# Performance work log

Measured on AMD Instinct MI355X. Metric: run time of the kernel, lower is better.

## Reference

```python
import jax, jax.numpy as jnp
import numpy as np

B, L = 128, 4096
H, RH, D, K = 128, 64, 64, 512  # num_hiddens, residual_hiddens, embedding_dim, num_embeddings
BETA = 0.25  # commitment_cost


def conv1d(x, w, b=None, stride=1, pad=0):
    # x: (N, C, W); w: (O, I, K) torch layout
    y = jax.lax.conv_general_dilated(x, w, (stride,), [(pad, pad)],
                                     dimension_numbers=('NCW', 'OIW', 'NCW'))
    return y if b is None else y + b[None, :, None]


def convT1d(x, w, b=None, stride=2, pad=1):
    # torch ConvTranspose1d weight layout (in, out, k)
    k = w.shape[-1]
    w_t = jnp.flip(w, -1).transpose(1, 0, 2)  # (out, in, k)
    y = jax.lax.conv_general_dilated(x, w_t, (1,), [(k - 1 - pad, k - 1 - pad)],
                                     lhs_dilation=(stride,),
                                     dimension_numbers=('NCW', 'OIW', 'NCW'))
    return y if b is None else y + b[None, :, None]


def res_stack(x, layers):
    for w1, w2 in layers:
        h = conv1d(jax.nn.relu(x), w1, None, 1, 1)
        h = conv1d(jax.nn.relu(h), w2, None, 1, 0)
        x = x + h
    return jax.nn.relu(x)


def _forward(x, enc_w1, enc_b1, enc_w2, enc_b2, enc_w3, enc_b3,
             enc_r1a, enc_r1b, enc_r2a, enc_r2b, pre_vq_w, pre_vq_b, codebook,
             dec_w1, dec_b1, dec_r1a, dec_r1b, dec_r2a, dec_r2b,
             dec_ct1_w, dec_ct1_b, dec_ct2_w, dec_ct2_b):
    # ---- Encoder (compression_factor == 4) ----
    h = x[:, None, :]                                   # (B, 1, L)
    h = jax.nn.relu(conv1d(h, enc_w1, enc_b1, 2, 1))    # (B, H/2, L/2)
    h = jax.nn.relu(conv1d(h, enc_w2, enc_b2, 2, 1))    # (B, H, L/4)
    h = conv1d(h, enc_w3, enc_b3, 1, 1)
    h = res_stack(h, [(enc_r1a, enc_r1b), (enc_r2a, enc_r2b)])
    z = conv1d(h, pre_vq_w, pre_vq_b, 1, 0)             # (B, D, T)

    # ---- Vector quantization ----
    zt = z.transpose(0, 2, 1)                           # (B, T, D)
    flat = zt.reshape(-1, D)                            # (BT, D)
    dists = (jnp.sum(flat * flat, 1, keepdims=True)
             - 2.0 * flat @ codebook.T
             + jnp.sum(codebook * codebook, 1))         # (BT, K)
    idx = jnp.argmin(dists, axis=1)                     # (BT,)
    q = codebook[idx].reshape(zt.shape)                 # (B, T, D)

    e_latent = jnp.mean((jax.lax.stop_gradient(q) - zt) ** 2)
    q_latent = jnp.mean((q - jax.lax.stop_gradient(zt)) ** 2)
    loss = q_latent + BETA * e_latent
    q_st = zt + jax.lax.stop_gradient(q - zt)           # straight-through

    counts = jnp.zeros((K,), flat.dtype).at[idx].add(1.0)
    probs = counts / idx.shape[0]
    perplexity = jnp.exp(-jnp.sum(probs * jnp.log(probs + 1e-10)))

    # ---- Decoder (compression_factor == 4) ----
    hd = q_st.transpose(0, 2, 1)                        # (B, D, T)
    hd = conv1d(hd, dec_w1, dec_b1, 1, 1)               # (B, H, T)
    hd = res_stack(hd, [(dec_r1a, dec_r1b), (dec_r2a, dec_r2b)])
    hd = jax.nn.relu(convT1d(hd, dec_ct1_w, dec_ct1_b)) # (B, H/2, 2T)
    hd = convT1d(hd, dec_ct2_w, dec_ct2_b)              # (B, 1, 4T)
    recon = jnp.squeeze(hd)                             # (B, L)
    return loss, recon, perplexity


def setup_inputs() -> dict:
    key = jax.random.key(0)
    ks = jax.random.split(key, 32)
    n = lambda i, shape, s=0.05: jax.random.normal(ks[i], shape, jnp.float32) * s
    inp = {
        'x': jax.random.normal(ks[0], (B, L), jnp.float32),
        'enc_w1': n(1, (H // 2, 1, 4)), 'enc_b1': jnp.zeros((H // 2,), jnp.float32),
        'enc_w2': n(2, (H, H // 2, 4)), 'enc_b2': jnp.zeros((H,), jnp.float32),
        'enc_w3': n(3, (H, H, 3)), 'enc_b3': jnp.zeros((H,), jnp.float32),
        'enc_r1a': n(4, (RH, H, 3)), 'enc_r1b': n(5, (H, RH, 1)),
        'enc_r2a': n(6, (RH, H, 3)), 'enc_r2b': n(7, (H, RH, 1)),
        'pre_vq_w': n(8, (D, H, 1)), 'pre_vq_b': jnp.zeros((D,), jnp.float32),
        'codebook': jax.random.uniform(ks[9], (K, D), jnp.float32, -1.0 / K, 1.0 / K),
        'dec_w1': n(10, (H, D, 3)), 'dec_b1': jnp.zeros((H,), jnp.float32),
        'dec_r1a': n(11, (RH, H, 3)), 'dec_r1b': n(12, (H, RH, 1)),
        'dec_r2a': n(13, (RH, H, 3)), 'dec_r2b': n(14, (H, RH, 1)),
        'dec_ct1_w': n(15, (H, H // 2, 4)), 'dec_ct1_b': jnp.zeros((H // 2,), jnp.float32),
        'dec_ct2_w': n(16, (H // 2, 1, 4)), 'dec_ct2_b': jnp.zeros((1,), jnp.float32),
    }
    return inp


def reference(x, enc_w1, enc_b1, enc_w2, enc_b2, enc_w3, enc_b3,
              enc_r1a, enc_r1b, enc_r2a, enc_r2b, pre_vq_w, pre_vq_b, codebook,
              dec_w1, dec_b1, dec_r1a, dec_r1b, dec_r2a, dec_r2b,
              dec_ct1_w, dec_ct1_b, dec_ct2_w, dec_ct2_b):
    return _forward(x, enc_w1, enc_b1, enc_w2, enc_b2, enc_w3, enc_b3,
                    enc_r1a, enc_r1b, enc_r2a, enc_r2b, pre_vq_w, pre_vq_b, codebook,
                    dec_w1, dec_b1, dec_r1a, dec_r1b, dec_r2a, dec_r2b,
                    dec_ct1_w, dec_ct1_b, dec_ct2_w, dec_ct2_b)
```

## Files before the change

### kernel.cpp

```cpp
#include <hip/hip_runtime.h>
#include <hip/hip_bf16.h>
#include <math.h>

using bf16 = __hip_bfloat16;
typedef __attribute__((ext_vector_type(4))) float f32x4;
typedef __attribute__((ext_vector_type(8))) short s16x8;

#define MFMA16(a,b,c) __builtin_amdgcn_mfma_f32_16x16x32_bf16((a),(b),(c),0,0,0)


__device__ inline float bf2f(unsigned short u) {
    union { float f; unsigned v; } c; c.v = ((unsigned)u) << 16; return c.f;
}
__device__ inline unsigned short bfbits(float f) {
    union { bf16 h; unsigned short u; } c; c.h = __float2bfloat16(f); return c.u;
}
__device__ inline s16x8 relu8(s16x8 v) {
#pragma unroll
    for (int j = 0; j < 8; ++j)
        v[j] = (short)(((unsigned short)v[j] & 0x8000u) ? 0 : (unsigned short)v[j]);
    return v;
}

enum { M_S1 = 0, M_S2 = 1, M_CT = 2 };

template<int CIN, int COUT, int NTAP, int MODE, bool RELU_IN, bool RELU_OUT,
         bool HAS_BIAS>
__global__ __launch_bounds__(256) void gconv_k(
    const bf16* __restrict__ in, const bf16* __restrict__ wt,
    const float* __restrict__ bias, bf16* __restrict__ out,
    int Lin, int Lout)
{
    constexpr int T  = (MODE == M_S2) ? 132 : ((MODE == M_CT) ? 66 : (NTAP == 3 ? 66 : 64));
    constexpr int NG = (MODE == M_CT) ? 2 : 1;
    constexpr int WL = (COUT == 128) ? 4 : 2;
    constexpr int KS = CIN / 32;
    constexpr int SOFF = (MODE == M_CT || NTAP == 3) ? -1 : 0;
    __shared__ bf16 sX[T * CIN];

    const int tid = threadIdx.x;
    const int b   = blockIdx.y;
    const int l0  = blockIdx.x * 64;
    const bf16* inb = in + (size_t)b * Lin * CIN;

    constexpr int CPR = CIN / 8;
    for (int i = tid; i < T * CPR; i += 256) {
        int t  = i / CPR;
        int c0 = (i - t * CPR) * 8;
        int g;
        if (MODE == M_S2) g = (t < 66) ? 2 * (l0 + t) : 2 * (l0 + t - 66) - 1;
        else              g = l0 + t + SOFF;
        s16x8 v = {};
        if (g >= 0 && g < Lin) v = *(const s16x8*)(inb + (size_t)g * CIN + c0);
        if (RELU_IN) v = relu8(v);
        int byte = ((t * CIN + c0) << 1) ^ ((t & 7) << 4);
        *(s16x8*)((char*)sX + byte) = v;
    }
    __syncthreads();

    const int lane = tid & 63;
    const int wid  = __builtin_amdgcn_readfirstlane(tid >> 6);
    const int co0  = (COUT == 128) ? wid * 32 : (wid & 1) * 32;
    const int lw0  = (COUT == 128) ? 0 : (wid >> 1) * 32;
    const int lr   = lane & 15;
    const int kg   = lane >> 4;

    f32x4 acc[NG][2][WL];
#pragma unroll
    for (int g = 0; g < NG; ++g)
#pragma unroll
        for (int cf = 0; cf < 2; ++cf)
#pragma unroll
            for (int lf = 0; lf < WL; ++lf)
                acc[g][cf][lf] = (f32x4){0.f, 0.f, 0.f, 0.f};

#pragma unroll
    for (int g = 0; g < NG; ++g) {
#pragma unroll
        for (int k = 0; k < NTAP; ++k) {
            int roff;
            if (MODE == M_S1)      roff = k;
            else if (MODE == M_S2) roff = (k == 0) ? 66 : (k == 1) ? 0 : (k == 2) ? 67 : 1;
            else                   roff = g + k;
            const bf16* Ab = wt + (size_t)(g * NTAP + k) * COUT * CIN;
#pragma unroll
            for (int ks = 0; ks < KS; ++ks) {
                s16x8 af[2];
#pragma unroll
                for (int cf = 0; cf < 2; ++cf)
                    af[cf] = *(const s16x8*)(Ab + (co0 + cf * 16 + lr) * CIN + ks * 32 + kg * 8);
                s16x8 bfr[WL];
#pragma unroll
                for (int lf = 0; lf < WL; ++lf) {
                    int t = roff + lw0 + lf * 16 + lr;
                    int byte = ((t * CIN + ks * 32 + kg * 8) << 1) ^ ((t & 7) << 4);
                    bfr[lf] = *(const s16x8*)((const char*)sX + byte);
                }
#pragma unroll
                for (int cf = 0; cf < 2; ++cf)
#pragma unroll
                    for (int lf = 0; lf < WL; ++lf)
                        acc[g][cf][lf] = MFMA16(af[cf], bfr[lf], acc[g][cf][lf]);
            }
        }
    }

#pragma unroll
    for (int g = 0; g < NG; ++g)
#pragma unroll
        for (int cf = 0; cf < 2; ++cf)
#pragma unroll
            for (int lf = 0; lf < WL; ++lf) {
                int cb0  = co0 + cf * 16 + kg * 4;
                int lcol = lw0 + lf * 16 + lr;
                int gcol = (MODE == M_CT) ? (2 * (l0 + lcol) + g) : (l0 + lcol);
                float r[4];
#pragma unroll
                for (int j = 0; j < 4; ++j) {
                    r[j] = acc[g][cf][lf][j];
                    if (HAS_BIAS) r[j] += bias[cb0 + j];
                    if (RELU_OUT) r[j] = fmaxf(r[j], 0.f);
                }
                bf16* po = out + ((size_t)b * Lout + gcol) * COUT + cb0;
                uint2 pk;
                pk.x = (unsigned)bfbits(r[0]) | ((unsigned)bfbits(r[1]) << 16);
                pk.y = (unsigned)bfbits(r[2]) | ((unsigned)bfbits(r[3]) << 16);
                *(uint2*)po = pk;
            }
}

template<bool RELU_OUT>
__global__ __launch_bounds__(256) void fres_k(
    const bf16* __restrict__ in, const bf16* __restrict__ w1t,
    const bf16* __restrict__ w2t, bf16* __restrict__ out)
{
    __shared__ bf16 sX[66 * 128];
    __shared__ bf16 sH[64 * 64];
    const int tid = threadIdx.x;
    const int b   = blockIdx.y;
    const int l0  = blockIdx.x * 64;
    const bf16* inb = in + (size_t)b * 1024 * 128;

    for (int i = tid; i < 66 * 16; i += 256) {
        int t = i >> 4, c0 = (i & 15) * 8;
        int g = l0 + t - 1;
        s16x8 v = {};
        if (g >= 0 && g < 1024) v = *(const s16x8*)(inb + (size_t)g * 128 + c0);
        int byte = ((t * 128 + c0) << 1) ^ ((t & 7) << 4);
        *(s16x8*)((char*)sX + byte) = v;
    }
    __syncthreads();

    const int lane = tid & 63;
    const int wid  = __builtin_amdgcn_readfirstlane(tid >> 6);
    const int lr   = lane & 15;
    const int kg   = lane >> 4;

    {
        const int co0 = (wid & 1) * 32;
        const int lw0 = (wid >> 1) * 32;
        f32x4 acc[2][2];
#pragma unroll
        for (int cf = 0; cf < 2; ++cf)
#pragma unroll
            for (int lf = 0; lf < 2; ++lf) acc[cf][lf] = (f32x4){0.f, 0.f, 0.f, 0.f};
#pragma unroll
        for (int k = 0; k < 3; ++k) {
            const bf16* Ab = w1t + (size_t)k * 64 * 128;
#pragma unroll
            for (int ks = 0; ks < 4; ++ks) {
                s16x8 af[2];
#pragma unroll
                for (int cf = 0; cf < 2; ++cf)
                    af[cf] = *(const s16x8*)(Ab + (co0 + cf * 16 + lr) * 128 + ks * 32 + kg * 8);
                s16x8 bfr[2];
#pragma unroll
                for (int lf = 0; lf < 2; ++lf) {
                    int t = k + lw0 + lf * 16 + lr;
                    int byte = ((t * 128 + ks * 32 + kg * 8) << 1) ^ ((t & 7) << 4);
                    bfr[lf] = relu8(*(const s16x8*)((const char*)sX + byte));
                }
#pragma unroll
                for (int cf = 0; cf < 2; ++cf)
#pragma unroll
                    for (int lf = 0; lf < 2; ++lf)
                        acc[cf][lf] = MFMA16(af[cf], bfr[lf], acc[cf][lf]);
            }
        }
#pragma unroll
        for (int cf = 0; cf < 2; ++cf)
#pragma unroll
            for (int lf = 0; lf < 2; ++lf) {
                int pos = lw0 + lf * 16 + lr;
                int ch  = co0 + cf * 16 + kg * 4;
                uint2 pk;
                pk.x = (unsigned)bfbits(fmaxf(acc[cf][lf][0], 0.f)) |
                       ((unsigned)bfbits(fmaxf(acc[cf][lf][1], 0.f)) << 16);
                pk.y = (unsigned)bfbits(fmaxf(acc[cf][lf][2], 0.f)) |
                       ((unsigned)bfbits(fmaxf(acc[cf][lf][3], 0.f)) << 16);
                int byte = ((pos * 64 + ch) << 1) ^ ((pos & 7) << 4);
                *(uint2*)((char*)sH + byte) = pk;
            }
    }
    __syncthreads();

    {
        const int co0 = wid * 32;
        f32x4 acc2[2][4];
#pragma unroll
        for (int cf = 0; cf < 2; ++cf)
#pragma unroll
            for (int lf = 0; lf < 4; ++lf) acc2[cf][lf] = (f32x4){0.f, 0.f, 0.f, 0.f};
#pragma unroll
        for (int ks = 0; ks < 2; ++ks) {
            s16x8 af[2];
#pragma unroll
            for (int cf = 0; cf < 2; ++cf)
                af[cf] = *(const s16x8*)(w2t + (size_t)(co0 + cf * 16 + lr) * 64 + ks * 32 + kg * 8);
            s16x8 bfr[4];
#pragma unroll
            for (int lf = 0; lf < 4; ++lf) {
                int t = lf * 16 + lr;
                int byte = ((t * 64 + ks * 32 + kg * 8) << 1) ^ ((t & 7) << 4);
                bfr[lf] = *(const s16x8*)((const char*)sH + byte);
            }
#pragma unroll
            for (int cf = 0; cf < 2; ++cf)
#pragma unroll
                for (int lf = 0; lf < 4; ++lf)
                    acc2[cf][lf] = MFMA16(af[cf], bfr[lf], acc2[cf][lf]);
        }
#pragma unroll
        for (int cf = 0; cf < 2; ++cf)
#pragma unroll
            for (int lf = 0; lf < 4; ++lf) {
                int cb0  = co0 + cf * 16 + kg * 4;
                int lcol = lf * 16 + lr;
                int tX   = lcol + 1;
                int rbyte = ((tX * 128 + cb0) << 1) ^ ((tX & 7) << 4);
                uint2 old = *(const uint2*)((const char*)sX + rbyte);
                float r[4];
                r[0] = acc2[cf][lf][0] + bf2f((unsigned short)(old.x & 0xffff));
                r[1] = acc2[cf][lf][1] + bf2f((unsigned short)(old.x >> 16));
                r[2] = acc2[cf][lf][2] + bf2f((unsigned short)(old.y & 0xffff));
                r[3] = acc2[cf][lf][3] + bf2f((unsigned short)(old.y >> 16));
                if (RELU_OUT)
#pragma unroll
                    for (int j = 0; j < 4; ++j) r[j] = fmaxf(r[j], 0.f);
                uint2 pk;
                pk.x = (unsigned)bfbits(r[0]) | ((unsigned)bfbits(r[1]) << 16);
                pk.y = (unsigned)bfbits(r[2]) | ((unsigned)bfbits(r[3]) << 16);
                *(uint2*)(out + ((size_t)b * 1024 + l0 + lcol) * 128 + cb0) = pk;
            }
    }
}

__global__ __launch_bounds__(256) void enc1_k(
    const float* __restrict__ x, const float* __restrict__ w,
    const float* __restrict__ bias, bf16* __restrict__ out)
{
    const int tid = threadIdx.x;
    const int b   = blockIdx.y;
    const int l   = blockIdx.x * 256 + tid;
    const float* xb = x + (size_t)b * 4096;
    float xv[4];
#pragma unroll
    for (int k = 0; k < 4; ++k) {
        int g = 2 * l - 1 + k;
        xv[k] = (g >= 0 && g < 4096) ? xb[g] : 0.f;
    }
    bf16* ob = out + ((size_t)b * 2048 + l) * 64;
#pragma unroll
    for (int c0 = 0; c0 < 64; c0 += 8) {
        union { unsigned short u[8]; s16x8 v; } pk;
#pragma unroll
        for (int j = 0; j < 8; ++j) {
            int co = c0 + j;
            float a = bias[co];
#pragma unroll
            for (int k = 0; k < 4; ++k) a = fmaf(xv[k], w[co * 4 + k], a);
            pk.u[j] = bfbits(fmaxf(a, 0.f));
        }
        *(s16x8*)(ob + c0) = pk.v;
    }
}

__global__ __launch_bounds__(256) void ct2_k(
    const bf16* __restrict__ in, const float* __restrict__ w,
    const float* __restrict__ bias, float* __restrict__ out)
{
    __shared__ bf16 sX[258 * 64];
    const int tid = threadIdx.x;
    const int b   = blockIdx.y;
    const int m0  = blockIdx.x * 256;
    const bf16* inb = in + (size_t)b * 2048 * 64;
    for (int i = tid; i < 258 * 8; i += 256) {
        int t = i >> 3, c0 = (i & 7) * 8;
        int g = m0 - 1 + t;
        s16x8 v = {};
        if (g >= 0 && g < 2048) v = *(const s16x8*)(inb + (size_t)g * 64 + c0);
        int byte = ((t * 64 + c0) << 1) ^ ((t & 7) << 4);
        *(s16x8*)((char*)sX + byte) = v;
    }
    __syncthreads();
    float e = bias[0], o = bias[0];
#pragma unroll
    for (int c0 = 0; c0 < 64; c0 += 8) {
        int t0 = tid, t1 = tid + 1, t2 = tid + 2;
        s16x8 vm1 = *(const s16x8*)((char*)sX + (((t0 * 64 + c0) << 1) ^ ((t0 & 7) << 4)));
        s16x8 v0  = *(const s16x8*)((char*)sX + (((t1 * 64 + c0) << 1) ^ ((t1 & 7) << 4)));
        s16x8 vp1 = *(const s16x8*)((char*)sX + (((t2 * 64 + c0) << 1) ^ ((t2 & 7) << 4)));
#pragma unroll
        for (int j = 0; j < 8; ++j) {
            int ci = c0 + j;
            float xm1 = bf2f((unsigned short)vm1[j]);
            float x0  = bf2f((unsigned short)v0[j]);
            float xp1 = bf2f((unsigned short)vp1[j]);
            e = fmaf(x0,  w[ci * 4 + 1], fmaf(xm1, w[ci * 4 + 3], e));
            o = fmaf(xp1, w[ci * 4 + 0], fmaf(x0,  w[ci * 4 + 2], o));
        }
    }
    int m = m0 + tid;
    out[(size_t)b * 4096 + 2 * m]     = e;
    out[(size_t)b * 4096 + 2 * m + 1] = o;
}

__global__ __launch_bounds__(256) void wx_k(
    const float* ew2, const float* ew3, const float* er1a, const float* er1b,
    const float* er2a, const float* er2b, const float* pvw, const float* dw1,
    const float* dr1a, const float* dr1b, const float* dr2a, const float* dr2b,
    const float* ct1w, bf16* wb)
{
    const int job = blockIdx.x;
    bf16* dst = wb + (size_t)job * 65536;
    const float* src; int CO, CI, K;
    switch (job) {
        case 0:  src = ew2;  CO = 128; CI = 64;  K = 4; break;
        case 1:  src = ew3;  CO = 128; CI = 128; K = 3; break;
        case 2:  src = er1a; CO = 64;  CI = 128; K = 3; break;
        case 3:  src = er1b; CO = 128; CI = 64;  K = 1; break;
        case 4:  src = er2a; CO = 64;  CI = 128; K = 3; break;
        case 5:  src = er2b; CO = 128; CI = 64;  K = 1; break;
        case 6:  src = pvw;  CO = 64;  CI = 128; K = 1; break;
        case 7:  src = dw1;  CO = 128; CI = 64;  K = 3; break;
        case 8:  src = dr1a; CO = 64;  CI = 128; K = 3; break;
        case 9:  src = dr1b; CO = 128; CI = 64;  K = 1; break;
        case 10: src = dr2a; CO = 64;  CI = 128; K = 3; break;
        case 11: src = dr2b; CO = 128; CI = 64;  K = 1; break;
        default: src = ct1w; CO = 64;  CI = 128; K = 4; break;
    }
    const int tot = CO * CI * K;
    for (int i = blockIdx.y * 256 + threadIdx.x; i < tot; i += gridDim.y * 256) {
        if (job < 12) {
            int k = i / (CO * CI); int r = i - k * CO * CI;
            int co = r / CI; int ci = r - co * CI;
            dst[i] = __float2bfloat16(src[((size_t)co * CI + ci) * K + k]);
        } else {
            const int TAP[4] = {3, 1, 2, 0};
            int g = i / (64 * 128); int r = i - g * 64 * 128;
            int co = r / 128; int ci = r - co * 128;
            dst[i] = __float2bfloat16(src[((size_t)ci * 64 + co) * 4 + TAP[g]]);
        }
    }
}

__global__ __launch_bounds__(256) void cbprep_k(
    const float* __restrict__ cb, bf16* __restrict__ cbh, bf16* __restrict__ cbl,
// ... 175 lines not shown
        float4 q1 = *(const float4*)(qp + c0 + 4);
        float qv[8] = {q0.x, q0.y, q0.z, q0.w, q1.x, q1.y, q1.z, q1.w};
        float zv[8] = {z0.x, z0.y, z0.z, z0.w, z1.x, z1.y, z1.z, z1.w};
        union { unsigned short u[8]; s16x8 v; } pk;
#pragma unroll
        for (int j = 0; j < 8; ++j) {
            float d = qv[j] - zv[j];
            lsum = fmaf(d, d, lsum);
            pk.u[j] = bfbits(qv[j]);
        }
        *(s16x8*)(q + (size_t)n * 64 + c0) = pk.v;
    }
#pragma unroll
    for (int off = 32; off > 0; off >>= 1) lsum += __shfl_down(lsum, off, 64);
    if ((tid & 63) == 0) sWS[tid >> 6] = lsum;
    __syncthreads();
    if (tid == 0) atomicAdd(loss_sum, sWS[0] + sWS[1] + sWS[2] + sWS[3]);
    float c0v = sHist[tid];       if (c0v != 0.f) atomicAdd(&counts[tid], c0v);
    float c1v = sHist[tid + 256]; if (c1v != 0.f) atomicAdd(&counts[tid + 256], c1v);
}

__global__ __launch_bounds__(512) void finalize_k(
    const float* __restrict__ counts, const float* __restrict__ loss_sum,
    float* __restrict__ d_out, int out_size)
{
    __shared__ float ws2[8];
    const int tid = threadIdx.x;
    float p = counts[tid] * (1.f / 131072.f);
    float e = p * logf(p + 1e-10f);
#pragma unroll
    for (int off = 32; off > 0; off >>= 1) e += __shfl_down(e, off, 64);
    const int lane = tid & 63, wid = tid >> 6;
    if (lane == 0) ws2[wid] = e;
    __syncthreads();
    if (tid == 0) {
        float s = 0.f;
        for (int i = 0; i < 8; ++i) s += ws2[i];
        d_out[0] = 1.25f * loss_sum[0] * (1.f / 8388608.f);
        d_out[out_size - 1] = expf(-s);
    }
}

extern "C" void kernel_launch(void* const* d_in, const int* in_sizes, int n_in,
                              void* d_out, int out_size, void* d_ws, size_t ws_size,
                              hipStream_t stream)
{
    const float* x        = (const float*)d_in[0];
    const float* enc_w1   = (const float*)d_in[1];
    const float* enc_b1   = (const float*)d_in[2];
    const float* enc_b2   = (const float*)d_in[4];
    const float* enc_b3   = (const float*)d_in[6];
    const float* pre_vq_b = (const float*)d_in[12];
    const float* cb       = (const float*)d_in[13];
    const float* dec_b1   = (const float*)d_in[15];
    const float* ct1_b    = (const float*)d_in[21];
    const float* ct2_w    = (const float*)d_in[22];
    const float* ct2_b    = (const float*)d_in[23];
    float* out = (float*)d_out;

    char* base = (char*)d_ws;
    bf16*  wb   = (bf16*)base;
    bf16*  Abf  = (bf16*)(base + ((size_t)2   << 20));
    bf16*  Bbf  = (bf16*)(base + ((size_t)40  << 20));
    bf16*  Qbf  = (bf16*)(base + ((size_t)78  << 20));
    bf16*  cbh  = (bf16*)(base + ((size_t)96  << 20));
    bf16*  cbl  = (bf16*)(base + ((size_t)96  << 20) + 65536);
    float* sc   = (float*)(base + ((size_t)96  << 20) + 131072);
    float* cnt  = sc + 512;
    float* lsum = cnt + 512;

    hipMemsetAsync(cnt, 0, 513 * sizeof(float), stream);

    dim3 blk(256);
    dim3 g16(16, 128);

    wx_k<<<dim3(13, 8), blk, 0, stream>>>(
        (const float*)d_in[3], (const float*)d_in[5], (const float*)d_in[7],
        (const float*)d_in[8], (const float*)d_in[9], (const float*)d_in[10],
        (const float*)d_in[11], (const float*)d_in[14], (const float*)d_in[16],
        (const float*)d_in[17], (const float*)d_in[18], (const float*)d_in[19],
        (const float*)d_in[20], wb);
    cbprep_k<<<2, blk, 0, stream>>>(cb, cbh, cbl, sc);

    enc1_k<<<dim3(8, 128), blk, 0, stream>>>(x, enc_w1, enc_b1, Abf);
    gconv_k<64,128,4,M_S2,false,true ,true ><<<g16, blk, 0, stream>>>(
        Abf, wb + 0 * 65536, enc_b2, Bbf, 2048, 1024);
    gconv_k<128,128,3,M_S1,false,false,true ><<<g16, blk, 0, stream>>>(
        Bbf, wb + 1 * 65536, enc_b3, Abf, 1024, 1024);
    fres_k<false><<<g16, blk, 0, stream>>>(Abf, wb + 2 * 65536, wb + 3 * 65536, Bbf);
    fres_k<true ><<<g16, blk, 0, stream>>>(Bbf, wb + 4 * 65536, wb + 5 * 65536, Abf);

    vqf_k<<<512, blk, 0, stream>>>(Abf, wb + 6 * 65536, pre_vq_b, cb,
                                   cbh, cbl, sc, Qbf, cnt, lsum);

    gconv_k<64,128,3,M_S1,false,false,true ><<<g16, blk, 0, stream>>>(
        Qbf, wb + 7 * 65536, dec_b1, Abf, 1024, 1024);
    fres_k<false><<<g16, blk, 0, stream>>>(Abf, wb + 8 * 65536, wb + 9 * 65536, Bbf);
    fres_k<true ><<<g16, blk, 0, stream>>>(Bbf, wb + 10 * 65536, wb + 11 * 65536, Abf);
    gconv_k<128,64,2,M_CT,false,true ,true ><<<g16, blk, 0, stream>>>(
        Abf, wb + 12 * 65536, ct1_b, Bbf, 1024, 2048);

    ct2_k<<<dim3(8, 128), blk, 0, stream>>>(Bbf, ct2_w, ct2_b, out + 1);
    finalize_k<<<1, 512, 0, stream>>>(cnt, lsum, out, out_size);
}
```

Measured before the change: 418.1 us.

## Fuse encoder and decoder conv/residual chains into halo-tiled megakernels

```diff
diff --git a/kernel.cpp b/kernel.cpp
--- a/kernel.cpp
+++ b/kernel.cpp
@@ -22,128 +22,23 @@
     return v;
 }
 
-enum { M_S1 = 0, M_S2 = 1, M_CT = 2 };
-
-template<int CIN, int COUT, int NTAP, int MODE, bool RELU_IN, bool RELU_OUT,
-         bool HAS_BIAS>
-__global__ __launch_bounds__(256) void gconv_k(
-    const bf16* __restrict__ in, const bf16* __restrict__ wt,
-    const float* __restrict__ bias, bf16* __restrict__ out,
-    int Lin, int Lout)
+__global__ __launch_bounds__(256) void encmid_k(
+    const bf16* __restrict__ in, const bf16* __restrict__ w3t,
+    const float* __restrict__ b3, const bf16* __restrict__ r1w1,
+    const bf16* __restrict__ r1w2, const bf16* __restrict__ r2w1,
+    const bf16* __restrict__ r2w2, bf16* __restrict__ out)
 {
-    constexpr int T  = (MODE == M_S2) ? 132 : ((MODE == M_CT) ? 66 : (NTAP == 3 ? 66 : 64));
-    constexpr int NG = (MODE == M_CT) ? 2 : 1;
-    constexpr int WL = (COUT == 128) ? 4 : 2;
-    constexpr int KS = CIN / 32;
-    constexpr int SOFF = (MODE == M_CT || NTAP == 3) ? -1 : 0;
-    __shared__ bf16 sX[T * CIN];
-
-    const int tid = threadIdx.x;
-    const int b   = blockIdx.y;
-    const int l0  = blockIdx.x * 64;
-    const bf16* inb = in + (size_t)b * Lin * CIN;
-
-    constexpr int CPR = CIN / 8;
-    for (int i = tid; i < T * CPR; i += 256) {
-        int t  = i / CPR;
-        int c0 = (i - t * CPR) * 8;
-        int g;
-        if (MODE == M_S2) g = (t < 66) ? 2 * (l0 + t) : 2 * (l0 + t - 66) - 1;
-        else              g = l0 + t + SOFF;
-        s16x8 v = {};
-        if (g >= 0 && g < Lin) v = *(const s16x8*)(inb + (size_t)g * CIN + c0);
-        if (RELU_IN) v = relu8(v);
-        int byte = ((t * CIN + c0) << 1) ^ ((t & 7) << 4);
-        *(s16x8*)((char*)sX + byte) = v;
-    }
-    __syncthreads();
-
-    const int lane = tid & 63;
-    const int wid  = __builtin_amdgcn_readfirstlane(tid >> 6);
-    const int co0  = (COUT == 128) ? wid * 32 : (wid & 1) * 32;
-    const int lw0  = (COUT == 128) ? 0 : (wid >> 1) * 32;
-    const int lr   = lane & 15;
-    const int kg   = lane >> 4;
-
-    f32x4 acc[NG][2][WL];
-#pragma unroll
-    for (int g = 0; g < NG; ++g)
-#pragma unroll
-        for (int cf = 0; cf < 2; ++cf)
-#pragma unroll
-            for (int lf = 0; lf < WL; ++lf)
-                acc[g][cf][lf] = (f32x4){0.f, 0.f, 0.f, 0.f};
-
-#pragma unroll
-    for (int g = 0; g < NG; ++g) {
-#pragma unroll
-        for (int k = 0; k < NTAP; ++k) {
-            int roff;
-            if (MODE == M_S1)      roff = k;
-            else if (MODE == M_S2) roff = (k == 0) ? 66 : (k == 1) ? 0 : (k == 2) ? 67 : 1;
-            else                   roff = g + k;
-            const bf16* Ab = wt + (size_t)(g * NTAP + k) * COUT * CIN;
-#pragma unroll
-            for (int ks = 0; ks < KS; ++ks) {
-                s16x8 af[2];
-#pragma unroll
-                for (int cf = 0; cf < 2; ++cf)
-                    af[cf] = *(const s16x8*)(Ab + (co0 + cf * 16 + lr) * CIN + ks * 32 + kg * 8);
-                s16x8 bfr[WL];
-#pragma unroll
-                for (int lf = 0; lf < WL; ++lf) {
-                    int t = roff + lw0 + lf * 16 + lr;
-                    int byte = ((t * CIN + ks * 32 + kg * 8) << 1) ^ ((t & 7) << 4);
-                    bfr[lf] = *(const s16x8*)((const char*)sX + byte);
-                }
-#pragma unroll
-                for (int cf = 0; cf < 2; ++cf)
-#pragma unroll
-                    for (int lf = 0; lf < WL; ++lf)
-                        acc[g][cf][lf] = MFMA16(af[cf], bfr[lf], acc[g][cf][lf]);
-            }
-        }
-    }
-
-#pragma unroll
-    for (int g = 0; g < NG; ++g)
-#pragma unroll
-        for (int cf = 0; cf < 2; ++cf)
-#pragma unroll
-            for (int lf = 0; lf < WL; ++lf) {
-                int cb0  = co0 + cf * 16 + kg * 4;
-                int lcol = lw0 + lf * 16 + lr;
-                int gcol = (MODE == M_CT) ? (2 * (l0 + lcol) + g) : (l0 + lcol);
-                float r[4];
-#pragma unroll
-                for (int j = 0; j < 4; ++j) {
-                    r[j] = acc[g][cf][lf][j];
-                    if (HAS_BIAS) r[j] += bias[cb0 + j];
-                    if (RELU_OUT) r[j] = fmaxf(r[j], 0.f);
-                }
-                bf16* po = out + ((size_t)b * Lout + gcol) * COUT + cb0;
-                uint2 pk;
-                pk.x = (unsigned)bfbits(r[0]) | ((unsigned)bfbits(r[1]) << 16);
-                pk.y = (unsigned)bfbits(r[2]) | ((unsigned)bfbits(r[3]) << 16);
-                *(uint2*)po = pk;
-            }
-}
-
-template<bool RELU_OUT>
-__global__ __launch_bounds__(256) void fres_k(
-    const bf16* __restrict__ in, const bf16* __restrict__ w1t,
-    const bf16* __restrict__ w2t, bf16* __restrict__ out)
-{
-    __shared__ bf16 sX[66 * 128];
-    __shared__ bf16 sH[64 * 64];
+    __shared__ bf16 sX[96 * 128];
+    __shared__ bf16 sY[80 * 128];
+    __shared__ bf16 sH[80 * 64];
     const int tid = threadIdx.x;
     const int b   = blockIdx.y;
     const int l0  = blockIdx.x * 64;
     const bf16* inb = in + (size_t)b * 1024 * 128;
 
-    for (int i = tid; i < 66 * 16; i += 256) {
+    for (int i = tid; i < 96 * 16; i += 256) {
         int t = i >> 4, c0 = (i & 15) * 8;
-        int g = l0 + t - 1;
+        int g = l0 - 16 + t;
         s16x8 v = {};
         if (g >= 0 && g < 1024) v = *(const s16x8*)(inb + (size_t)g * 128 + c0);
         int byte = ((t * 128 + c0) << 1) ^ ((t & 7) << 4);
@@ -155,134 +50,519 @@
     const int wid  = __builtin_amdgcn_readfirstlane(tid >> 6);
     const int lr   = lane & 15;
     const int kg   = lane >> 4;
+    const f32x4 zf4 = {0.f, 0.f, 0.f, 0.f};
 
     {
-        const int co0 = (wid & 1) * 32;
-        const int lw0 = (wid >> 1) * 32;
-        f32x4 acc[2][2];
+        const int co0 = wid * 32;
+        f32x4 acc[2][5];
 #pragma unroll
         for (int cf = 0; cf < 2; ++cf)
 #pragma unroll
-            for (int lf = 0; lf < 2; ++lf) acc[cf][lf] = (f32x4){0.f, 0.f, 0.f, 0.f};
+            for (int lf = 0; lf < 5; ++lf) acc[cf][lf] = zf4;
 #pragma unroll
         for (int k = 0; k < 3; ++k) {
-            const bf16* Ab = w1t + (size_t)k * 64 * 128;
+            const bf16* Ab = w3t + (size_t)k * 128 * 128;
 #pragma unroll
             for (int ks = 0; ks < 4; ++ks) {
                 s16x8 af[2];
 #pragma unroll
                 for (int cf = 0; cf < 2; ++cf)
                     af[cf] = *(const s16x8*)(Ab + (co0 + cf * 16 + lr) * 128 + ks * 32 + kg * 8);
-                s16x8 bfr[2];
-#pragma unroll
-                for (int lf = 0; lf < 2; ++lf) {
-                    int t = k + lw0 + lf * 16 + lr;
-                    int byte = ((t * 128 + ks * 32 + kg * 8) << 1) ^ ((t & 7) << 4);
-                    bfr[lf] = relu8(*(const s16x8*)((const char*)sX + byte));
+                s16x8 bfr[5];
+#pragma unroll
+                for (int lf = 0; lf < 5; ++lf) {
+                    int tx = lf * 16 + lr + 7 + k;
+                    int byte = ((tx * 128 + ks * 32 + kg * 8) << 1) ^ ((tx & 7) << 4);
+                    bfr[lf] = *(const s16x8*)((const char*)sX + byte);
                 }
 #pragma unroll
                 for (int cf = 0; cf < 2; ++cf)
 #pragma unroll
-                    for (int lf = 0; lf < 2; ++lf)
+                    for (int lf = 0; lf < 5; ++lf)
                         acc[cf][lf] = MFMA16(af[cf], bfr[lf], acc[cf][lf]);
             }
         }
 #pragma unroll
         for (int cf = 0; cf < 2; ++cf)
 #pragma unroll
-            for (int lf = 0; lf < 2; ++lf) {
-                int pos = lw0 + lf * 16 + lr;
-                int ch  = co0 + cf * 16 + kg * 4;
-                uint2 pk;
-                pk.x = (unsigned)bfbits(fmaxf(acc[cf][lf][0], 0.f)) |
-                       ((unsigned)bfbits(fmaxf(acc[cf][lf][1], 0.f)) << 16);
-                pk.y = (unsigned)bfbits(fmaxf(acc[cf][lf][2], 0.f)) |
-                       ((unsigned)bfbits(fmaxf(acc[cf][lf][3], 0.f)) << 16);
-                int byte = ((pos * 64 + ch) << 1) ^ ((pos & 7) << 4);
-                *(uint2*)((char*)sH + byte) = pk;
-            }
-    }
-    __syncthreads();
-
-    {
-        const int co0 = wid * 32;
-        f32x4 acc2[2][4];
-#pragma unroll
-        for (int cf = 0; cf < 2; ++cf)
-#pragma unroll
-            for (int lf = 0; lf < 4; ++lf) acc2[cf][lf] = (f32x4){0.f, 0.f, 0.f, 0.f};
-#pragma unroll
-        for (int ks = 0; ks < 2; ++ks) {
-            s16x8 af[2];
-#pragma unroll
-            for (int cf = 0; cf < 2; ++cf)
-                af[cf] = *(const s16x8*)(w2t + (size_t)(co0 + cf * 16 + lr) * 64 + ks * 32 + kg * 8);
-            s16x8 bfr[4];
-#pragma unroll
-            for (int lf = 0; lf < 4; ++lf) {
-                int t = lf * 16 + lr;
-                int byte = ((t * 64 + ks * 32 + kg * 8) << 1) ^ ((t & 7) << 4);
-                bfr[lf] = *(const s16x8*)((const char*)sH + byte);
-            }
-#pragma unroll
-            for (int cf = 0; cf < 2; ++cf)
-#pragma unroll
-                for (int lf = 0; lf < 4; ++lf)
-                    acc2[cf][lf] = MFMA16(af[cf], bfr[lf], acc2[cf][lf]);
-        }
-#pragma unroll
-        for (int cf = 0; cf < 2; ++cf)
-#pragma unroll
-            for (int lf = 0; lf < 4; ++lf) {
-                int cb0  = co0 + cf * 16 + kg * 4;
-                int lcol = lf * 16 + lr;
-                int tX   = lcol + 1;
-                int rbyte = ((tX * 128 + cb0) << 1) ^ ((tX & 7) << 4);
-                uint2 old = *(const uint2*)((const char*)sX + rbyte);
+            for (int lf = 0; lf < 5; ++lf) {
+                int row = lf * 16 + lr;
+                int p   = l0 - 8 + row;
+                int cb0 = co0 + cf * 16 + kg * 4;
+                bool ok = (p >= 0 && p < 1024);
                 float r[4];
-                r[0] = acc2[cf][lf][0] + bf2f((unsigned short)(old.x & 0xffff));
-                r[1] = acc2[cf][lf][1] + bf2f((unsigned short)(old.x >> 16));
-                r[2] = acc2[cf][lf][2] + bf2f((unsigned short)(old.y & 0xffff));
-                r[3] = acc2[cf][lf][3] + bf2f((unsigned short)(old.y >> 16));
-                if (RELU_OUT)
-#pragma unroll
-                    for (int j = 0; j < 4; ++j) r[j] = fmaxf(r[j], 0.f);
+#pragma unroll
+                for (int j = 0; j < 4; ++j)
+                    r[j] = ok ? (acc[cf][lf][j] + b3[cb0 + j]) : 0.f;
                 uint2 pk;
                 pk.x = (unsigned)bfbits(r[0]) | ((unsigned)bfbits(r[1]) << 16);
                 pk.y = (unsigned)bfbits(r[2]) | ((unsigned)bfbits(r[3]) << 16);
-                *(uint2*)(out + ((size_t)b * 1024 + l0 + lcol) * 128 + cb0) = pk;
-            }
-    }
-}
-
-__global__ __launch_bounds__(256) void enc1_k(
-    const float* __restrict__ x, const float* __restrict__ w,
-    const float* __restrict__ bias, bf16* __restrict__ out)
+                int byte = ((row * 128 + cb0) << 1) ^ ((row & 7) << 4);
+                *(uint2*)((char*)sY + byte) = pk;
+            }
+    }
+    __syncthreads();
+
+#pragma unroll 1
+    for (int blk = 0; blk < 2; ++blk) {
+        const bf16* w1 = blk ? r2w1 : r1w1;
+        {
+            const int co0 = wid * 16;
+            f32x4 acc[5];
+#pragma unroll
+            for (int lf = 0; lf < 5; ++lf) acc[lf] = zf4;
+#pragma unroll
+            for (int k = 0; k < 3; ++k) {
+                const bf16* Ab = w1 + (size_t)k * 64 * 128;
+#pragma unroll
+                for (int ks = 0; ks < 4; ++ks) {
+                    s16x8 a = *(const s16x8*)(Ab + (co0 + lr) * 128 + ks * 32 + kg * 8);
+                    s16x8 bfr[5];
+#pragma unroll
+                    for (int lf = 0; lf < 5; ++lf) {
+                        int ry = lf * 16 + lr + k - 1;
+                        ry = (ry < 0) ? 0 : (ry > 79 ? 79 : ry);
+                        int byte = ((ry * 128 + ks * 32 + kg * 8) << 1) ^ ((ry & 7) << 4);
+                        bfr[lf] = relu8(*(const s16x8*)((const char*)sY + byte));
+                    }
+#pragma unroll
+                    for (int lf = 0; lf < 5; ++lf)
+                        acc[lf] = MFMA16(a, bfr[lf], acc[lf]);
+                }
+            }
+#pragma unroll
+            for (int lf = 0; lf < 5; ++lf) {
+                int row = lf * 16 + lr;
+                int ch0 = co0 + kg * 4;
+                uint2 pk;
+                pk.x = (unsigned)bfbits(fmaxf(acc[lf][0], 0.f)) |
+                       ((unsigned)bfbits(fmaxf(acc[lf][1], 0.f)) << 16);
+                pk.y = (unsigned)bfbits(fmaxf(acc[lf][2], 0.f)) |
+                       ((unsigned)bfbits(fmaxf(acc[lf][3], 0.f)) << 16);
+                int byte = ((row * 64 + ch0) << 1) ^ ((row & 7) << 4);
+                *(uint2*)((char*)sH + byte) = pk;
+            }
+        }
+        __syncthreads();
+
+        if (blk == 0) {
+            const int co0 = wid * 32;
+            f32x4 acc[2][5];
+#pragma unroll
+            for (int cf = 0; cf < 2; ++cf)
+#pragma unroll
+                for (int lf = 0; lf < 5; ++lf) acc[cf][lf] = zf4;
+#pragma unroll
+            for (int ks = 0; ks < 2; ++ks) {
+                s16x8 af[2];
+#pragma unroll
+                for (int cf = 0; cf < 2; ++cf)
+                    af[cf] = *(const s16x8*)(r1w2 + (size_t)(co0 + cf * 16 + lr) * 64 + ks * 32 + kg * 8);
+                s16x8 bfr[5];
+#pragma unroll
+                for (int lf = 0; lf < 5; ++lf) {
+                    int row = lf * 16 + lr;
+                    int byte = ((row * 64 + ks * 32 + kg * 8) << 1) ^ ((row & 7) << 4);
+                    bfr[lf] = *(const s16x8*)((const char*)sH + byte);
+                }
+#pragma unroll
+                for (int cf = 0; cf < 2; ++cf)
+#pragma unroll
+                    for (int lf = 0; lf < 5; ++lf)
+                        acc[cf][lf] = MFMA16(af[cf], bfr[lf], acc[cf][lf]);
+            }
+#pragma unroll
+            for (int cf = 0; cf < 2; ++cf)
+#pragma unroll
+                for (int lf = 0; lf < 5; ++lf) {
+                    int row = lf * 16 + lr;
+                    int p   = l0 - 8 + row;
+                    int cb0 = co0 + cf * 16 + kg * 4;
+                    int byte = ((row * 128 + cb0) << 1) ^ ((row & 7) << 4);
+                    uint2 old = *(const uint2*)((const char*)sY + byte);
+                    bool ok = (p >= 0 && p < 1024);
+                    float r[4];
+                    r[0] = acc[cf][lf][0] + bf2f((unsigned short)(old.x & 0xffff));
+                    r[1] = acc[cf][lf][1] + bf2f((unsigned short)(old.x >> 16));
+                    r[2] = acc[cf][lf][2] + bf2f((unsigned short)(old.y & 0xffff));
+                    r[3] = acc[cf][lf][3] + bf2f((unsigned short)(old.y >> 16));
+                    uint2 pk;
+                    pk.x = ok ? ((unsigned)bfbits(r[0]) | ((unsigned)bfbits(r[1]) << 16)) : 0u;
+                    pk.y = ok ? ((unsigned)bfbits(r[2]) | ((unsigned)bfbits(r[3]) << 16)) : 0u;
+                    *(uint2*)((char*)sY + byte) = pk;
+                }
+            __syncthreads();
+        } else {
+            const int co0 = wid * 32;
+            f32x4 acc[2][4];
+#pragma unroll
+            for (int cf = 0; cf < 2; ++cf)
+#pragma unroll
+                for (int lf = 0; lf < 4; ++lf) acc[cf][lf] = zf4;
+#pragma unroll
+            for (int ks = 0; ks < 2; ++ks) {
+                s16x8 af[2];
+#pragma unroll
+                for (int cf = 0; cf < 2; ++cf)
+                    af[cf] = *(const s16x8*)(r2w2 + (size_t)(co0 + cf * 16 + lr) * 64 + ks * 32 + kg * 8);
+                s16x8 bfr[4];
+#pragma unroll
+                for (int lf = 0; lf < 4; ++lf) {
+                    int row = 8 + lf * 16 + lr;
+                    int byte = ((row * 64 + ks * 32 + kg * 8) << 1) ^ ((row & 7) << 4);
+                    bfr[lf] = *(const s16x8*)((const char*)sH + byte);
+                }
+#pragma unroll
+                for (int cf = 0; cf < 2; ++cf)
+#pragma unroll
+                    for (int lf = 0; lf < 4; ++lf)
+                        acc[cf][lf] = MFMA16(af[cf], bfr[lf], acc[cf][lf]);
+            }
+#pragma unroll
+            for (int cf = 0; cf < 2; ++cf)
+#pragma unroll
+                for (int lf = 0; lf < 4; ++lf) {
+                    int row = 8 + lf * 16 + lr;
+                    int cb0 = co0 + cf * 16 + kg * 4;
+                    int byte = ((row * 128 + cb0) << 1) ^ ((row & 7) << 4);
+                    uint2 old = *(const uint2*)((const char*)sY + byte);
+                    float r[4];
+                    r[0] = fmaxf(acc[cf][lf][0] + bf2f((unsigned short)(old.x & 0xffff)), 0.f);
+                    r[1] = fmaxf(acc[cf][lf][1] + bf2f((unsigned short)(old.x >> 16)), 0.f);
+                    r[2] = fmaxf(acc[cf][lf][2] + bf2f((unsigned short)(old.y & 0xffff)), 0.f);
+                    r[3] = fmaxf(acc[cf][lf][3] + bf2f((unsigned short)(old.y >> 16)), 0.f);
+                    uint2 pk;
+                    pk.x = (unsigned)bfbits(r[0]) | ((unsigned)bfbits(r[1]) << 16);
+                    pk.y = (unsigned)bfbits(r[2]) | ((unsigned)bfbits(r[3]) << 16);
+                    *(uint2*)(out + ((size_t)b * 1024 + l0 + lf * 16 + lr) * 128 + cb0) = pk;
+                }
+        }
+    }
+}
+
+__global__ __launch_bounds__(256) void decmid_k(
+    const bf16* __restrict__ qin, const bf16* __restrict__ dw1,
+    const float* __restrict__ db1, const bf16* __restrict__ r1w1,
+    const bf16* __restrict__ r1w2, const bf16* __restrict__ r2w1,
+    const bf16* __restrict__ r2w2, const bf16* __restrict__ ct1w,
+    const float* __restrict__ ct1b, bf16* __restrict__ out)
 {
+    __shared__ bf16 sQ[96 * 64];
+    __shared__ bf16 sY[80 * 128];
+    __shared__ bf16 sH[80 * 64];
     const int tid = threadIdx.x;
     const int b   = blockIdx.y;
-    const int l   = blockIdx.x * 256 + tid;
+    const int l0  = blockIdx.x * 64;
+    const bf16* inb = qin + (size_t)b * 1024 * 64;
+
+    for (int i = tid; i < 96 * 8; i += 256) {
+        int t = i >> 3, c0 = (i & 7) * 8;
+        int g = l0 - 16 + t;
+        s16x8 v = {};
+        if (g >= 0 && g < 1024) v = *(const s16x8*)(inb + (size_t)g * 64 + c0);
+        int byte = ((t * 64 + c0) << 1) ^ ((t & 7) << 4);
+        *(s16x8*)((char*)sQ + byte) = v;
+    }
+    __syncthreads();
+
+    const int lane = tid & 63;
+    const int wid  = __builtin_amdgcn_readfirstlane(tid >> 6);
+    const int lr   = lane & 15;
+    const int kg   = lane >> 4;
+    const f32x4 zf4 = {0.f, 0.f, 0.f, 0.f};
+
+    {
+        const int co0 = wid * 32;
+        f32x4 acc[2][5];
+#pragma unroll
+        for (int cf = 0; cf < 2; ++cf)
+#pragma unroll
+            for (int lf = 0; lf < 5; ++lf) acc[cf][lf] = zf4;
+#pragma unroll
+        for (int k = 0; k < 3; ++k) {
+            const bf16* Ab = dw1 + (size_t)k * 128 * 64;
+#pragma unroll
+            for (int ks = 0; ks < 2; ++ks) {
+                s16x8 af[2];
+#pragma unroll
+                for (int cf = 0; cf < 2; ++cf)
+                    af[cf] = *(const s16x8*)(Ab + (co0 + cf * 16 + lr) * 64 + ks * 32 + kg * 8);
+                s16x8 bfr[5];
+#pragma unroll
+                for (int lf = 0; lf < 5; ++lf) {
+                    int tx = lf * 16 + lr + 7 + k;
+                    int byte = ((tx * 64 + ks * 32 + kg * 8) << 1) ^ ((tx & 7) << 4);
+                    bfr[lf] = *(const s16x8*)((const char*)sQ + byte);
+                }
+#pragma unroll
+                for (int cf = 0; cf < 2; ++cf)
+#pragma unroll
+                    for (int lf = 0; lf < 5; ++lf)
+                        acc[cf][lf] = MFMA16(af[cf], bfr[lf], acc[cf][lf]);
+            }
+        }
+#pragma unroll
+        for (int cf = 0; cf < 2; ++cf)
+#pragma unroll
+            for (int lf = 0; lf < 5; ++lf) {
+                int row = lf * 16 + lr;
+                int p   = l0 - 8 + row;
+                int cb0 = co0 + cf * 16 + kg * 4;
+                bool ok = (p >= 0 && p < 1024);
+                float r[4];
+#pragma unroll
+                for (int j = 0; j < 4; ++j)
+                    r[j] = ok ? (acc[cf][lf][j] + db1[cb0 + j]) : 0.f;
+                uint2 pk;
+                pk.x = (unsigned)bfbits(r[0]) | ((unsigned)bfbits(r[1]) << 16);
+                pk.y = (unsigned)bfbits(r[2]) | ((unsigned)bfbits(r[3]) << 16);
+                int byte = ((row * 128 + cb0) << 1) ^ ((row & 7) << 4);
+                *(uint2*)((char*)sY + byte) = pk;
+            }
+    }
+    __syncthreads();
+
+#pragma unroll 1
+    for (int blk = 0; blk < 2; ++blk) {
+        const bf16* w1 = blk ? r2w1 : r1w1;
+        const bf16* w2 = blk ? r2w2 : r1w2;
+        {
+            const int co0 = wid * 16;
+            f32x4 acc[5];
+#pragma unroll
+            for (int lf = 0; lf < 5; ++lf) acc[lf] = zf4;
+#pragma unroll
+            for (int k = 0; k < 3; ++k) {
+                const bf16* Ab = w1 + (size_t)k * 64 * 128;
+#pragma unroll
+                for (int ks = 0; ks < 4; ++ks) {
+                    s16x8 a = *(const s16x8*)(Ab + (co0 + lr) * 128 + ks * 32 + kg * 8);
+                    s16x8 bfr[5];
+#pragma unroll
+                    for (int lf = 0; lf < 5; ++lf) {
+                        int ry = lf * 16 + lr + k - 1;
+                        ry = (ry < 0) ? 0 : (ry > 79 ? 79 : ry);
+                        int byte = ((ry * 128 + ks * 32 + kg * 8) << 1) ^ ((ry & 7) << 4);
+                        bfr[lf] = relu8(*(const s16x8*)((const char*)sY + byte));
+                    }
+#pragma unroll
+                    for (int lf = 0; lf < 5; ++lf)
+                        acc[lf] = MFMA16(a, bfr[lf], acc[lf]);
+                }
+            }
+#pragma unroll
+            for (int lf = 0; lf < 5; ++lf) {
+                int row = lf * 16 + lr;
+                int ch0 = co0 + kg * 4;
+                uint2 pk;
+                pk.x = (unsigned)bfbits(fmaxf(acc[lf][0], 0.f)) |
+                       ((unsigned)bfbits(fmaxf(acc[lf][1], 0.f)) << 16);
+                pk.y = (unsigned)bfbits(fmaxf(acc[lf][2], 0.f)) |
+                       ((unsigned)bfbits(fmaxf(acc[lf][3], 0.f)) << 16);
+                int byte = ((row * 64 + ch0) << 1) ^ ((row & 7) << 4);
+                *(uint2*)((char*)sH + byte) = pk;
+            }
+        }
+        __syncthreads();
+        {
+            const int co0 = wid * 32;
+            f32x4 acc[2][5];
+#pragma unroll
+            for (int cf = 0; cf < 2; ++cf)
+#pragma unroll
+                for (int lf = 0; lf < 5; ++lf) acc[cf][lf] = zf4;
+#pragma unroll
+            for (int ks = 0; ks < 2; ++ks) {
+                s16x8 af[2];
+#pragma unroll
+                for (int cf = 0; cf < 2; ++cf)
+                    af[cf] = *(const s16x8*)(w2 + (size_t)(co0 + cf * 16 + lr) * 64 + ks * 32 + kg * 8);
+                s16x8 bfr[5];
+#pragma unroll
+                for (int lf = 0; lf < 5; ++lf) {
+                    int row = lf * 16 + lr;
+                    int byte = ((row * 64 + ks * 32 + kg * 8) << 1) ^ ((row & 7) << 4);
+                    bfr[lf] = *(const s16x8*)((const char*)sH + byte);
+                }
+#pragma unroll
+                for (int cf = 0; cf < 2; ++cf)
+#pragma unroll
+                    for (int lf = 0; lf < 5; ++lf)
+                        acc[cf][lf] = MFMA16(af[cf], bfr[lf], acc[cf][lf]);
+            }
+#pragma unroll
+            for (int cf = 0; cf < 2; ++cf)
+#pragma unroll
+                for (int lf = 0; lf < 5; ++lf) {
+                    int row = lf * 16 + lr;
+                    int p   = l0 - 8 + row;
+                    int cb0 = co0 + cf * 16 + kg * 4;
+                    int byte = ((row * 128 + cb0) << 1) ^ ((row & 7) << 4);
+                    uint2 old = *(const uint2*)((const char*)sY + byte);
+                    bool ok = (p >= 0 && p < 1024);
+                    float r[4];
+                    r[0] = acc[cf][lf][0] + bf2f((unsigned short)(old.x & 0xffff));
+                    r[1] = acc[cf][lf][1] + bf2f((unsigned short)(old.x >> 16));
+                    r[2] = acc[cf][lf][2] + bf2f((unsigned short)(old.y & 0xffff));
+                    r[3] = acc[cf][lf][3] + bf2f((unsigned short)(old.y >> 16));
+                    if (blk == 1)
+#pragma unroll
+                        for (int j = 0; j < 4; ++j) r[j] = fmaxf(r[j], 0.f);
+                    uint2 pk;
+                    pk.x = ok ? ((unsigned)bfbits(r[0]) | ((unsigned)bfbits(r[1]) << 16)) : 0u;
+                    pk.y = ok ? ((unsigned)bfbits(r[2]) | ((unsigned)bfbits(r[3]) << 16)) : 0u;
+                    *(uint2*)((char*)sY + byte) = pk;
+                }
+        }
+        __syncthreads();
+    }
+
+    {
+        const int co0 = (wid & 1) * 32;
+        const int mh  = wid >> 1;
+        f32x4 acc[2][2][2];
+#pragma unroll
+        for (int g = 0; g < 2; ++g)
+#pragma unroll
+            for (int cf = 0; cf < 2; ++cf)
+#pragma unroll
+                for (int j = 0; j < 2; ++j) acc[g][cf][j] = zf4;
+#pragma unroll
+        for (int g = 0; g < 2; ++g)
+#pragma unroll
+            for (int k = 0; k < 2; ++k) {
+                const bf16* Ab = ct1w + (size_t)(g * 2 + k) * 64 * 128;
+                const int doff = (g == 0) ? (k - 1) : k;
+#pragma unroll
+                for (int ks = 0; ks < 4; ++ks) {
+                    s16x8 af[2];
+#pragma unroll
+                    for (int cf = 0; cf < 2; ++cf)
+                        af[cf] = *(const s16x8*)(Ab + (co0 + cf * 16 + lr) * 128 + ks * 32 + kg * 8);
+                    s16x8 bfr[2];
+#pragma unroll
+                    for (int j = 0; j < 2; ++j) {
+                        int ty = 8 + (mh * 2 + j) * 16 + lr + doff;
+                        int byte = ((ty * 128 + ks * 32 + kg * 8) << 1) ^ ((ty & 7) << 4);
+                        bfr[j] = *(const s16x8*)((const char*)sY + byte);
+                    }
+#pragma unroll
+                    for (int cf = 0; cf < 2; ++cf)
+#pragma unroll
+                        for (int j = 0; j < 2; ++j)
+                            acc[g][cf][j] = MFMA16(af[cf], bfr[j], acc[g][cf][j]);
+                }
+            }
+#pragma unroll
+        for (int g = 0; g < 2; ++g)
+#pragma unroll
+            for (int cf = 0; cf < 2; ++cf)
+#pragma unroll
+                for (int j = 0; j < 2; ++j) {
+                    int m   = (mh * 2 + j) * 16 + lr;
+                    int cb0 = co0 + cf * 16 + kg * 4;
+                    float r[4];
+#pragma unroll
+                    for (int jj = 0; jj < 4; ++jj)
+                        r[jj] = fmaxf(acc[g][cf][j][jj] + ct1b[cb0 + jj], 0.f);
+                    uint2 pk;
+                    pk.x = (unsigned)bfbits(r[0]) | ((unsigned)bfbits(r[1]) << 16);
+                    pk.y = (unsigned)bfbits(r[2]) | ((unsigned)bfbits(r[3]) << 16);
+                    *(uint2*)(out + ((size_t)b * 2048 + 2 * (l0 + m) + g) * 64 + cb0) = pk;
+                }
+    }
+}
+
+__global__ __launch_bounds__(256) void enc12_k(
+    const float* __restrict__ x, const float* __restrict__ w1,
+    const float* __restrict__ b1, const bf16* __restrict__ w2t,
+    const float* __restrict__ b2, bf16* __restrict__ out)
+{
+    __shared__ float sXf[268];
+    __shared__ float sW1[256];
+    __shared__ float sB1[64];
+    __shared__ bf16 sX[132 * 64];
+    const int tid = threadIdx.x;
+    const int b   = blockIdx.y;
+    const int l0  = blockIdx.x * 64;
     const float* xb = x + (size_t)b * 4096;
-    float xv[4];
+
+    for (int i = tid; i < 266; i += 256) {
+        int g = 4 * l0 - 3 + i;
+        sXf[i] = (g >= 0 && g < 4096) ? xb[g] : 0.f;
+    }
+    if (tid < 256) sW1[tid] = w1[tid];
+    if (tid < 64)  sB1[tid] = b1[tid];
+    __syncthreads();
+
+    for (int i = tid; i < 132 * 64; i += 256) {
+        int t = i >> 6, c = i & 63;
+        int p = (t < 66) ? 2 * (l0 + t) : 2 * (l0 + t - 66) - 1;
+        float v = 0.f;
+        if (p >= 0 && p < 2048) {
+            int xi = 2 * p - 4 * l0 + 2;
+            float a = sB1[c];
+#pragma unroll
+            for (int k = 0; k < 4; ++k) a = fmaf(sXf[xi + k], sW1[c * 4 + k], a);
+            v = fmaxf(a, 0.f);
+        }
+        int byte = ((t * 64 + c) << 1) ^ ((t & 7) << 4);
+        *(bf16*)((char*)sX + byte) = __float2bfloat16(v);
+    }
+    __syncthreads();
+
+    const int lane = tid & 63;
+    const int wid  = __builtin_amdgcn_readfirstlane(tid >> 6);
+    const int co0  = wid * 32;
+    const int lr   = lane & 15;
+    const int kg   = lane >> 4;
+
+    f32x4 acc[2][4];
+#pragma unroll
+    for (int cf = 0; cf < 2; ++cf)
+#pragma unroll
+        for (int lf = 0; lf < 4; ++lf) acc[cf][lf] = (f32x4){0.f, 0.f, 0.f, 0.f};
+
 #pragma unroll
     for (int k = 0; k < 4; ++k) {
-        int g = 2 * l - 1 + k;
-        xv[k] = (g >= 0 && g < 4096) ? xb[g] : 0.f;
-    }
-    bf16* ob = out + ((size_t)b * 2048 + l) * 64;
-#pragma unroll
-    for (int c0 = 0; c0 < 64; c0 += 8) {
-        union { unsigned short u[8]; s16x8 v; } pk;
-#pragma unroll
-        for (int j = 0; j < 8; ++j) {
-            int co = c0 + j;
-            float a = bias[co];
-#pragma unroll
-            for (int k = 0; k < 4; ++k) a = fmaf(xv[k], w[co * 4 + k], a);
-            pk.u[j] = bfbits(fmaxf(a, 0.f));
-        }
-        *(s16x8*)(ob + c0) = pk.v;
-    }
+        const int roff = (k == 0) ? 66 : (k == 1) ? 0 : (k == 2) ? 67 : 1;
+        const bf16* Ab = w2t + (size_t)k * 128 * 64;
+#pragma unroll
+        for (int ks = 0; ks < 2; ++ks) {
+            s16x8 af[2];
+#pragma unroll
+            for (int cf = 0; cf < 2; ++cf)
+                af[cf] = *(const s16x8*)(Ab + (co0 + cf * 16 + lr) * 64 + ks * 32 + kg * 8);
+            s16x8 bfr[4];
+#pragma unroll
+            for (int lf = 0; lf < 4; ++lf) {
+                int t = roff + lf * 16 + lr;
+                int byte = ((t * 64 + ks * 32 + kg * 8) << 1) ^ ((t & 7) << 4);
+                bfr[lf] = *(const s16x8*)((const char*)sX + byte);
+            }
+#pragma unroll
+            for (int cf = 0; cf < 2; ++cf)
+#pragma unroll
+                for (int lf = 0; lf < 4; ++lf)
+                    acc[cf][lf] = MFMA16(af[cf], bfr[lf], acc[cf][lf]);
+        }
+    }
+
+#pragma unroll
+    for (int cf = 0; cf < 2; ++cf)
+#pragma unroll
+        for (int lf = 0; lf < 4; ++lf) {
+            int cb0  = co0 + cf * 16 + kg * 4;
+            int lcol = lf * 16 + lr;
+            float r[4];
+#pragma unroll
+            for (int j = 0; j < 4; ++j)
+                r[j] = fmaxf(acc[cf][lf][j] + b2[cb0 + j], 0.f);
+            uint2 pk;
+            pk.x = (unsigned)bfbits(r[0]) | ((unsigned)bfbits(r[1]) << 16);
+            pk.y = (unsigned)bfbits(r[2]) | ((unsigned)bfbits(r[3]) << 16);
+            *(uint2*)(out + ((size_t)b * 1024 + l0 + lcol) * 128 + cb0) = pk;
+        }
 }
 
 __global__ __launch_bounds__(256) void ct2_k(
@@ -624,23 +904,16 @@
         (const float*)d_in[20], wb);
     cbprep_k<<<2, blk, 0, stream>>>(cb, cbh, cbl, sc);
 
-    enc1_k<<<dim3(8, 128), blk, 0, stream>>>(x, enc_w1, enc_b1, Abf);
-    gconv_k<64,128,4,M_S2,false,true ,true ><<<g16, blk, 0, stream>>>(
-        Abf, wb + 0 * 65536, enc_b2, Bbf, 2048, 1024);
-    gconv_k<128,128,3,M_S1,false,false,true ><<<g16, blk, 0, stream>>>(
-        Bbf, wb + 1 * 65536, enc_b3, Abf, 1024, 1024);
-    fres_k<false><<<g16, blk, 0, stream>>>(Abf, wb + 2 * 65536, wb + 3 * 65536, Bbf);
-    fres_k<true ><<<g16, blk, 0, stream>>>(Bbf, wb + 4 * 65536, wb + 5 * 65536, Abf);
+    enc12_k<<<g16, blk, 0, stream>>>(x, enc_w1, enc_b1, wb + 0 * 65536, enc_b2, Bbf);
+    encmid_k<<<g16, blk, 0, stream>>>(Bbf, wb + 1 * 65536, enc_b3,
+        wb + 2 * 65536, wb + 3 * 65536, wb + 4 * 65536, wb + 5 * 65536, Abf);
 
     vqf_k<<<512, blk, 0, stream>>>(Abf, wb + 6 * 65536, pre_vq_b, cb,
                                    cbh, cbl, sc, Qbf, cnt, lsum);
 
-    gconv_k<64,128,3,M_S1,false,false,true ><<<g16, blk, 0, stream>>>(
-        Qbf, wb + 7 * 65536, dec_b1, Abf, 1024, 1024);
-    fres_k<false><<<g16, blk, 0, stream>>>(Abf, wb + 8 * 65536, wb + 9 * 65536, Bbf);
-    fres_k<true ><<<g16, blk, 0, stream>>>(Bbf, wb + 10 * 65536, wb + 11 * 65536, Abf);
-    gconv_k<128,64,2,M_CT,false,true ,true ><<<g16, blk, 0, stream>>>(
-        Abf, wb + 12 * 65536, ct1_b, Bbf, 1024, 2048);
+    decmid_k<<<g16, blk, 0, stream>>>(Qbf, wb + 7 * 65536, dec_b1,
+        wb + 8 * 65536, wb + 9 * 65536, wb + 10 * 65536, wb + 11 * 65536,
+        wb + 12 * 65536, ct1_b, Bbf);
 
     ct2_k<<<dim3(8, 128), blk, 0, stream>>>(Bbf, ct2_w, ct2_b, out + 1);
     finalize_k<<<1, 512, 0, stream>>>(cnt, lsum, out, out_size);
```

Result: faster. 358.6 us (-14.2%).
